# Kernel tuning notes

Measured on AMD Instinct MI355X. Metric: run time of the kernel, lower is better.

Reference implementation:

```python
import jax, jax.numpy as jnp
import numpy as np

B, T, D, HD = 8, 2048, 1024, 64

def setup_inputs() -> dict:
    key = jax.random.key(0)
    k1, k2, k3, k4 = jax.random.split(key, 4)
    x = jax.random.normal(k1, (B, T, D), dtype=jnp.float32)
    Wq = jax.random.normal(k2, (D, HD), dtype=jnp.float32) * (D ** -0.5)
    Wk = jax.random.normal(k3, (D, HD), dtype=jnp.float32) * (D ** -0.5)
    Wv = jax.random.normal(k4, (D, HD), dtype=jnp.float32) * (D ** -0.5)
    return {"x": x, "Wq": Wq, "Wk": Wk, "Wv": Wv}

def reference(x, Wq, Wk, Wv):
    # x: [B,T,D]; projections: [D,HD]
    q = jnp.einsum('btd,dh->bth', x, Wq)
    k = jnp.einsum('btd,dh->bth', x, Wk)
    v = jnp.einsum('btd,dh->bth', x, Wv)
    hd = q.shape[-1]
    scores = jnp.einsum('bth,bsh->bts', q, k) * (hd ** -0.5)  # [B,T,T]
    t = scores.shape[-1]
    causal = jnp.tril(jnp.ones((t, t), dtype=bool))
    scores = jnp.where(causal, scores, -jnp.inf)
    w = jax.nn.softmax(scores, axis=-1)
    # dropout p=0.0 (eval) -> identity
    return jnp.einsum('bts,bsh->bth', w, v)
```

## Files before the change

kernel.cpp:

```cpp
#include <hip/hip_runtime.h>
#include <hip/hip_bf16.h>
#include <stdint.h>

#define NB 8
#define TT 2048
#define DD 1024
#define HDIM 64

typedef __bf16 bf16x8 __attribute__((ext_vector_type(8)));
typedef float f32x4 __attribute__((ext_vector_type(4)));
typedef ushort u16x4 __attribute__((ext_vector_type(4)));

static_assert(sizeof(bf16x8) == 16, "bf16x8 must be 16 bytes");

__device__ inline ushort f2bf_bits(float f) {
    __hip_bfloat16 h = __float2bfloat16(f);
    return *reinterpret_cast<ushort*>(&h);
}
__device__ inline float bfbits2f(ushort u) {
    unsigned v = ((unsigned)u) << 16;
    return __builtin_bit_cast(float, v);
}
__device__ inline bf16x8 ldb8(const ushort* p) {
    return *reinterpret_cast<const bf16x8*>(p);
}

typedef __attribute__((address_space(3))) uint32_t lds_u32;
typedef const __attribute__((address_space(1))) uint32_t glb_u32;
__device__ inline void gl_lds16(const void* g, void* l) {
    __builtin_amdgcn_global_load_lds((glb_u32*)g, (lds_u32*)l, 16, 0, 0);
}

#define WCNT_VM2   0xF72
#define WCNT_VM5   0xF75
#define WCNT_LGKM0 0xC07F

__device__ inline int probe_f32(const ushort* x) {
    int lane = threadIdx.x & 63;
    int wild = 0;
    #pragma unroll
    for (int j = 0; j < 4; ++j) {
        ushort u = x[(lane * 4 + j) * 32];
        int e = (u >> 7) & 0xFF;
        wild += (e >= 0xC0);
    }
    unsigned long long m = __ballot(wild > 0);
    return __popcll(m) > 8;
}

__global__ __launch_bounds__(256) void k_wt(const ushort* __restrict__ x,
                                            const void* __restrict__ Wq,
                                            const void* __restrict__ Wk,
                                            const void* __restrict__ Wv,
                                            ushort* __restrict__ Wt) {
    int f32m = probe_f32(x);
    int idx = blockIdx.x * 256 + threadIdx.x;
    int mat = idx >> 16;
    int rem = idx & 65535;
    int d = rem >> 6;
    int h = rem & 63;
    const void* W = (mat == 0) ? Wq : (mat == 1) ? Wk : Wv;
    float v;
    if (f32m) v = ((const float*)W)[rem];
    else      v = bfbits2f(((const ushort*)W)[rem]);
    if (mat == 0) v *= 0.18033688011112042f;
    int n    = mat * 64 + h;
    int nt   = n >> 4, ncol = n & 15;
    int kk   = d >> 6, ks = (d >> 5) & 1, qd = (d >> 3) & 3, e = d & 7;
    int f    = nt * 2 + ks;
    Wt[((size_t)(kk * 24 + f)) * 512 + (qd * 16 + ncol) * 8 + e] = f2bf_bits(v);
}

template <int F32M>
__device__ inline void proj_body(const void* __restrict__ xv,
                                 const ushort* __restrict__ Wt,
                                 ushort* __restrict__ Qw,
                                 ushort* __restrict__ Kw,
                                 ushort* __restrict__ V2,
                                 ushort* Bf, ushort* Afb) {
    int tid  = threadIdx.x;
    int w    = tid >> 6;
    int lane = tid & 63;
    int quad = lane >> 4;
    int col  = lane & 15;
    int mtw  = w >> 2;
    int nh   = w & 3;
    int m0   = blockIdx.x * 64;

    const float*  xf = (const float*)xv;
    const ushort* xb = (const ushort*)xv;

    auto stageB = [&](int buf, int kkk) {
        int kk24 = (kkk >> 6) * 24;
        #pragma unroll
        for (int j = 0; j < 3; ++j) {
            int f = w * 3 + j;
            gl_lds16(Wt + ((size_t)(kk24 + f)) * 512 + lane * 8,
                     Bf + ((size_t)buf * 24 + f) * 512);
        }
    };

    int arow  = m0 + w * 8 + (lane >> 3);
    int amt_s = w >> 1;
    int colp  = (w & 1) * 8 + (lane >> 3);
    f32x4 arf[2];
    u16x4 arb[2];
    auto loadA = [&](int kkk) {
        #pragma unroll
        for (int i = 0; i < 2; ++i) {
            int c = (lane & 7) + i * 8;
            if (F32M) arf[i] = *reinterpret_cast<const f32x4*>(xf + (size_t)arow * DD + kkk + c * 4);
            else      arb[i] = *reinterpret_cast<const u16x4*>(xb + (size_t)arow * DD + kkk + c * 4);
        }
    };
    auto writeA = [&](int q) {
        #pragma unroll
        for (int i = 0; i < 2; ++i) {
            int c  = (lane & 7) + i * 8;
            int ks = i;
            int qd = (c & 7) >> 1;
            int e0 = (c & 1) * 4;
            u16x4 v;
            if (F32M) {
                #pragma unroll
                for (int j = 0; j < 4; ++j) v[j] = f2bf_bits(arf[i][j]);
            } else {
                v = arb[i];
            }
            *reinterpret_cast<u16x4*>(Afb + ((size_t)q * 16 + amt_s * 2 + ks) * 512
                                      + (qd * 16 + colp) * 8 + e0) = v;
        }
    };

    f32x4 acc[2][3];
    #pragma unroll
    for (int i = 0; i < 2; ++i)
        #pragma unroll
        for (int j = 0; j < 3; ++j) acc[i][j] = (f32x4){0.f, 0.f, 0.f, 0.f};

    loadA(0);
    stageB(0, 0);
    writeA(0);
    __builtin_amdgcn_s_waitcnt(WCNT_LGKM0);

    for (int t = 0; t < 16; ++t) {
        int p   = t & 1;
        int kn1 = (t + 1 < 16) ? (t + 1) * 64 : 960;
        loadA(kn1);
        stageB(p ^ 1, kn1);
        __builtin_amdgcn_s_waitcnt(WCNT_VM5);
        __builtin_amdgcn_s_barrier();

        #pragma unroll
        for (int ks = 0; ks < 2; ++ks) {
            bf16x8 a0 = ldb8(Afb + ((size_t)p * 16 + (mtw * 2 + 0) * 2 + ks) * 512 + lane * 8);
            bf16x8 a1 = ldb8(Afb + ((size_t)p * 16 + (mtw * 2 + 1) * 2 + ks) * 512 + lane * 8);
            #pragma unroll
            for (int j = 0; j < 3; ++j) {
                int nt = nh * 3 + j;
                bf16x8 b = ldb8(Bf + ((size_t)p * 24 + nt * 2 + ks) * 512 + lane * 8);
                acc[0][j] = __builtin_amdgcn_mfma_f32_16x16x32_bf16(a0, b, acc[0][j], 0, 0, 0);
                acc[1][j] = __builtin_amdgcn_mfma_f32_16x16x32_bf16(a1, b, acc[1][j], 0, 0, 0);
            }
        }
        writeA(p ^ 1);
        __builtin_amdgcn_s_waitcnt(WCNT_LGKM0);
        __builtin_amdgcn_s_barrier();
    }

    #pragma unroll
    for (int mloc = 0; mloc < 2; ++mloc) {
        #pragma unroll
        for (int j = 0; j < 3; ++j) {
            int nt  = nh * 3 + j;
            int mat = nt >> 2;
            int h   = (nt & 3) * 16 + col;
            if (mat == 2) {
                int row0 = m0 + mtw * 32 + mloc * 16 + quad * 4;
                int bb   = row0 >> 11;
                int t0   = row0 & (TT - 1);
                u16x4 v;
                #pragma unroll
                for (int r = 0; r < 4; ++r) v[r] = f2bf_bits(acc[mloc][j][r]);
                *reinterpret_cast<u16x4*>(V2 + (size_t)bb * HDIM * TT
                                          + (size_t)(t0 >> 5) * 2048
                                          + h * 32 + (t0 & 31)) = v;
            } else {
                ushort* outp = (mat == 0) ? Qw : Kw;
                #pragma unroll
                for (int r = 0; r < 4; ++r) {
                    int row = m0 + mtw * 32 + mloc * 16 + quad * 4 + r;
                    outp[(size_t)row * HDIM + h] = f2bf_bits(acc[mloc][j][r]);
                }
            }
        }
    }
}

__global__ __launch_bounds__(512, 4) void k_proj(const void* __restrict__ xv,
                                                 const ushort* __restrict__ Wt,
                                                 ushort* __restrict__ Qw,
                                                 ushort* __restrict__ Kw,
                                                 ushort* __restrict__ V2) {
    __shared__ ushort Bf[2 * 24 * 512];
    __shared__ ushort Afb[2 * 16 * 512];
    if (probe_f32((const ushort*)xv)) proj_body<1>(xv, Wt, Qw, Kw, V2, Bf, Afb);
    else                              proj_body<0>(xv, Wt, Qw, Kw, V2, Bf, Afb);
}

__global__ __launch_bounds__(256) void k_attn(const ushort* __restrict__ Qw,
                                              const ushort* __restrict__ Kw,
                                              const ushort* __restrict__ V2w,
                                              ushort* __restrict__ Po,
                                              float* __restrict__ Pl) {
    int w    = threadIdx.x >> 6;
    int lane = threadIdx.x & 63;
    int quad = lane >> 4;
    int col  = lane & 15;
    int bid  = blockIdx.x;
    int b    = bid & 7;
    int idx  = 79 - (bid >> 3);
    int c, g;
    if (idx < 32)      { c = 0; g = idx; }
    else if (idx < 56) { c = 1; g = idx - 24; }
    else if (idx < 72) { c = 2; g = idx - 40; }
    else               { c = 3; g = idx - 48; }
    int qb = 4 * g + w;
    int m0 = qb * 16;
    int Bq = (qb < 32) ? qb : (qb < 64) ? 2*qb - 32 : (qb < 96) ? 3*qb - 96 : 4*qb - 192;
    int pid = b * 320 + Bq + c;

    const ushort* Qb  = Qw  + (size_t)b * TT * HDIM;
    const ushort* Kb  = Kw  + (size_t)b * TT * HDIM;
    const ushort* V2b = V2w + (size_t)b * HDIM * TT;

    __shared__ ushort KVb[2][4096];
    __shared__ __hip_bfloat16 Pls[4][16][40];

    auto stageKV = [&](int buf, int s) {
        #pragma unroll
        for (int j = 0; j < 2; ++j) {
            int i = w * 2 + j;
            const ushort* gp;
            if (i < 4) {
                int row = i * 8 + (lane >> 3);
                int cg  = (lane & 7) ^ (lane >> 3);
                gp = Kb + (size_t)(s + row) * HDIM + cg * 8;
            } else {
                int w3 = (lane & 7) ^ (lane >> 3);
                int d  = (i - 4) * 16 + 2 * (lane >> 3) + (w3 >> 2);
                int cg = w3 & 3;
                gp = V2b + (size_t)(s >> 5) * 2048 + d * 32 + cg * 8;
            }
            gl_lds16(gp, &KVb[buf][i * 512]);
        }
    };

    int cb7  = col & 7;
    int vlow = (quad + 4 * (col & 1)) ^ ((col >> 1) & 7);
    auto kslot = [&](int rb, int half) {
        return ((rb + col) * 8 + ((half * 4 + quad) ^ cb7)) * 8;
    };
    auto vslot = [&](int vg) {
        return 2048 + ((vg * 8 + (col >> 1)) * 8 + vlow) * 8;
    };

    bf16x8 qf0 = ldb8(Qb + (size_t)(m0 + col) * HDIM + quad * 8);
    bf16x8 qf1 = ldb8(Qb + (size_t)(m0 + col) * HDIM + 32 + quad * 8);

    f32x4 o0 = {0.f,0.f,0.f,0.f};
    f32x4 o1 = {0.f,0.f,0.f,0.f};
    f32x4 o2 = {0.f,0.f,0.f,0.f};
    f32x4 o3 = {0.f,0.f,0.f,0.f};
    float rsum[4] = {0.f, 0.f, 0.f, 0.f};

    const int start = c * 512;
    const int end   = min(start + 512, 64 * g + 64);

    stageKV(0, start);
    for (int s0 = start; s0 < end; s0 += 32) {
        int p  = ((s0 - start) >> 5) & 1;
        int sn = (s0 + 32 < end) ? s0 + 32 : s0;
        stageKV(p ^ 1, sn);
        __builtin_amdgcn_s_waitcnt(WCNT_VM2);
        __builtin_amdgcn_s_barrier();

        if (s0 < m0 + 16) {
            bf16x8 ck0l = ldb8(&KVb[p][kslot(0,  0)]);
            bf16x8 ck0h = ldb8(&KVb[p][kslot(0,  1)]);
            bf16x8 ck1l = ldb8(&KVb[p][kslot(16, 0)]);
            bf16x8 ck1h = ldb8(&KVb[p][kslot(16, 1)]);

            f32x4 S0 = {0.f,0.f,0.f,0.f};
            f32x4 S1 = {0.f,0.f,0.f,0.f};
            S0 = __builtin_amdgcn_mfma_f32_16x16x32_bf16(qf0, ck0l, S0, 0, 0, 0);
            S0 = __builtin_amdgcn_mfma_f32_16x16x32_bf16(qf1, ck0h, S0, 0, 0, 0);
            S1 = __builtin_amdgcn_mfma_f32_16x16x32_bf16(qf0, ck1l, S1, 0, 0, 0);
            S1 = __builtin_amdgcn_mfma_f32_16x16x32_bf16(qf1, ck1h, S1, 0, 0, 0);

            #pragma unroll
            for (int r = 0; r < 4; ++r) {
                int trow = m0 + quad * 4 + r;
                float aa = (s0 + col      > trow) ? -1e30f : S0[r];
                float dd = (s0 + 16 + col > trow) ? -1e30f : S1[r];
                float p0 = exp2f(aa);
                float p1 = exp2f(dd);
                rsum[r] += p0 + p1;
                Pls[w][quad * 4 + r][col]      = __float2bfloat16(p0);
                Pls[w][quad * 4 + r][16 + col] = __float2bfloat16(p1);
            }
            bf16x8 pf = *reinterpret_cast<const bf16x8*>(&Pls[w][col][quad * 8]);

            bf16x8 cv0 = ldb8(&KVb[p][vslot(0)]);
            bf16x8 cv1 = ldb8(&KVb[p][vslot(1)]);
            bf16x8 cv2 = ldb8(&KVb[p][vslot(2)]);
            bf16x8 cv3 = ldb8(&KVb[p][vslot(3)]);
            o0 = __builtin_amdgcn_mfma_f32_16x16x32_bf16(pf, cv0, o0, 0, 0, 0);
            o1 = __builtin_amdgcn_mfma_f32_16x16x32_bf16(pf, cv1, o1, 0, 0, 0);
            o2 = __builtin_amdgcn_mfma_f32_16x16x32_bf16(pf, cv2, o2, 0, 0, 0);
            o3 = __builtin_amdgcn_mfma_f32_16x16x32_bf16(pf, cv3, o3, 0, 0, 0);
        }
        __builtin_amdgcn_s_waitcnt(WCNT_LGKM0);
        __builtin_amdgcn_s_barrier();
    }

    #pragma unroll
    for (int off = 1; off < 16; off <<= 1) {
        #pragma unroll
        for (int r = 0; r < 4; ++r)
            rsum[r] += __shfl_xor(rsum[r], off, 64);
    }

    ushort* pb = Po + (size_t)pid * 1024;
    #pragma unroll
    for (int r = 0; r < 4; ++r) {
        int row = quad * 4 + r;
        pb[row * 64 + 0*16 + col] = f2bf_bits(o0[r]);
        pb[row * 64 + 1*16 + col] = f2bf_bits(o1[r]);
        pb[row * 64 + 2*16 + col] = f2bf_bits(o2[r]);
        pb[row * 64 + 3*16 + col] = f2bf_bits(o3[r]);
        if (col == 0) Pl[pid * 16 + row] = rsum[r];
    }
}

__global__ __launch_bounds__(256) void k_merge(const ushort* __restrict__ x,
                                               const ushort* __restrict__ Po,
                                               const float* __restrict__ Pl,
                                               void* __restrict__ outv) {
    int f32m = probe_f32(x);
    int wid  = blockIdx.x * 4 + (threadIdx.x >> 6);
    int lane = threadIdx.x & 63;
    int row  = lane >> 2;
    int g    = lane & 3;
    int b    = wid >> 7;
    int qb   = wid & 127;
    int nch  = (qb >> 5) + 1;
    int Bq   = (qb < 32) ? qb : (qb < 64) ? 2*qb - 32 : (qb < 96) ? 3*qb - 96 : 4*qb - 192;
    int pid0 = b * 320 + Bq;

    float L = 0.f;
    #pragma unroll
    for (int c = 0; c < 4; ++c)
        if (c < nch) L += Pl[(pid0 + c) * 16 + row];
    float inv = 1.0f / L;

    float o[16];
    #pragma unroll
    for (int j = 0; j < 16; ++j) o[j] = 0.f;
    #pragma unroll
    for (int c = 0; c < 4; ++c) {
        if (c < nch) {
            const ushort* p = Po + (size_t)(pid0 + c) * 1024 + row * 64 + g * 16;
            bf16x8 v0 = ldb8(p);
            bf16x8 v1 = ldb8(p + 8);
            #pragma unroll
            for (int j = 0; j < 8; ++j) {
                o[j]     += (float)v0[j];
                o[8 + j] += (float)v1[j];
            }
        }
    }

    size_t obase = ((size_t)b * TT + qb * 16 + row) * HDIM + g * 16;
    if (f32m) {
        float* ob = (float*)outv + obase;
        #pragma unroll
        for (int j = 0; j < 16; ++j) ob[j] = o[j] * inv;
    } else {
        ushort* ob = (ushort*)outv + obase;
        #pragma unroll
        for (int j = 0; j < 16; ++j) ob[j] = f2bf_bits(o[j] * inv);
    }
}

extern "C" void kernel_launch(void* const* d_in, const int* in_sizes, int n_in,
                              void* d_out, int out_size, void* d_ws, size_t ws_size,
                              hipStream_t stream) {
    const ushort* x = (const ushort*)d_in[0];
    ushort* Wt  = (ushort*)d_ws;
    ushort* Qw  = Wt + 3 * HDIM * DD;
    ushort* Kw  = Qw + (size_t)NB * TT * HDIM;
    ushort* V2  = Kw + (size_t)NB * TT * HDIM;
    ushort* Po  = V2 + (size_t)NB * TT * HDIM;
    float*  Pl  = (float*)(Po + (size_t)2560 * 1024);

    k_wt   <<<768, 256, 0, stream>>>(x, d_in[1], d_in[2], d_in[3], Wt);
    k_proj <<<256, 512, 0, stream>>>(d_in[0], Wt, Qw, Kw, V2);
    k_attn <<<640, 256, 0, stream>>>(Qw, Kw, V2, Po, Pl);
    k_merge<<<256, 256, 0, stream>>>(x, Po, Pl, d_out);
}
```

Baseline: 142.4 us.

## Fuse split-KV merge into attention kernel via atomic last-block reduction

Removes the separate merge kernel launch. Query blocks that have a single KV chunk now normalize and write the output directly. Multi-chunk blocks write their partials, bump an atomic counter, and the last-arriving wave reduces all chunks and writes the final output. This saves one kernel launch and the partial round-trip for single-chunk rows, at the cost of threadfences, atomics and a serialized tail reduction inside the attention kernel. The counters are zeroed in the weight-transform kernel.

```diff
diff --git a/kernel.cpp b/kernel.cpp
--- a/kernel.cpp
+++ b/kernel.cpp
@@ -52,9 +52,11 @@
                                             const void* __restrict__ Wq,
                                             const void* __restrict__ Wk,
                                             const void* __restrict__ Wv,
-                                            ushort* __restrict__ Wt) {
+                                            ushort* __restrict__ Wt,
+                                            int* __restrict__ cnt) {
     int f32m = probe_f32(x);
     int idx = blockIdx.x * 256 + threadIdx.x;
+    if (idx < 1024) cnt[idx] = 0;
     int mat = idx >> 16;
     int rem = idx & 65535;
     int d = rem >> 6;
@@ -208,11 +210,15 @@
     else                              proj_body<0>(xv, Wt, Qw, Kw, V2, Bf, Afb);
 }
 
-__global__ __launch_bounds__(256) void k_attn(const ushort* __restrict__ Qw,
+__global__ __launch_bounds__(256) void k_attn(const ushort* __restrict__ xp,
+                                              const ushort* __restrict__ Qw,
                                               const ushort* __restrict__ Kw,
                                               const ushort* __restrict__ V2w,
                                               ushort* __restrict__ Po,
-                                              float* __restrict__ Pl) {
+                                              float* __restrict__ Pl,
+                                              int* __restrict__ cnt,
+                                              void* __restrict__ outv) {
+    int f32m = probe_f32(xp);
     int w    = threadIdx.x >> 6;
     int lane = threadIdx.x & 63;
     int quad = lane >> 4;
@@ -227,8 +233,10 @@
     else               { c = 3; g = idx - 48; }
     int qb = 4 * g + w;
     int m0 = qb * 16;
+    int nch = (qb >> 5) + 1;
     int Bq = (qb < 32) ? qb : (qb < 64) ? 2*qb - 32 : (qb < 96) ? 3*qb - 96 : 4*qb - 192;
-    int pid = b * 320 + Bq + c;
+    int pid0 = b * 320 + Bq;
+    int pid  = pid0 + c;
 
     const ushort* Qb  = Qw  + (size_t)b * TT * HDIM;
     const ushort* Kb  = Kw  + (size_t)b * TT * HDIM;
@@ -331,65 +339,77 @@
             rsum[r] += __shfl_xor(rsum[r], off, 64);
     }
 
-    ushort* pb = Po + (size_t)pid * 1024;
-    #pragma unroll
-    for (int r = 0; r < 4; ++r) {
-        int row = quad * 4 + r;
-        pb[row * 64 + 0*16 + col] = f2bf_bits(o0[r]);
-        pb[row * 64 + 1*16 + col] = f2bf_bits(o1[r]);
-        pb[row * 64 + 2*16 + col] = f2bf_bits(o2[r]);
-        pb[row * 64 + 3*16 + col] = f2bf_bits(o3[r]);
-        if (col == 0) Pl[pid * 16 + row] = rsum[r];
-    }
-}
-
-__global__ __launch_bounds__(256) void k_merge(const ushort* __restrict__ x,
-                                               const ushort* __restrict__ Po,
-                                               const float* __restrict__ Pl,
-                                               void* __restrict__ outv) {
-    int f32m = probe_f32(x);
-    int wid  = blockIdx.x * 4 + (threadIdx.x >> 6);
-    int lane = threadIdx.x & 63;
-    int row  = lane >> 2;
-    int g    = lane & 3;
-    int b    = wid >> 7;
-    int qb   = wid & 127;
-    int nch  = (qb >> 5) + 1;
-    int Bq   = (qb < 32) ? qb : (qb < 64) ? 2*qb - 32 : (qb < 96) ? 3*qb - 96 : 4*qb - 192;
-    int pid0 = b * 320 + Bq;
-
-    float L = 0.f;
-    #pragma unroll
-    for (int c = 0; c < 4; ++c)
-        if (c < nch) L += Pl[(pid0 + c) * 16 + row];
-    float inv = 1.0f / L;
-
-    float o[16];
-    #pragma unroll
-    for (int j = 0; j < 16; ++j) o[j] = 0.f;
-    #pragma unroll
-    for (int c = 0; c < 4; ++c) {
-        if (c < nch) {
-            const ushort* p = Po + (size_t)(pid0 + c) * 1024 + row * 64 + g * 16;
-            bf16x8 v0 = ldb8(p);
-            bf16x8 v1 = ldb8(p + 8);
+    if (nch == 1) {
+        size_t base = ((size_t)b * TT + (size_t)m0) * HDIM;
+        #pragma unroll
+        for (int r = 0; r < 4; ++r) {
+            float inv = 1.0f / rsum[r];
+            size_t ro = base + (size_t)(quad * 4 + r) * HDIM;
+            if (f32m) {
+                float* ob = (float*)outv;
+                ob[ro + 0*16 + col] = o0[r] * inv;
+                ob[ro + 1*16 + col] = o1[r] * inv;
+                ob[ro + 2*16 + col] = o2[r] * inv;
+                ob[ro + 3*16 + col] = o3[r] * inv;
+            } else {
+                ushort* ob = (ushort*)outv;
+                ob[ro + 0*16 + col] = f2bf_bits(o0[r] * inv);
+                ob[ro + 1*16 + col] = f2bf_bits(o1[r] * inv);
+                ob[ro + 2*16 + col] = f2bf_bits(o2[r] * inv);
+                ob[ro + 3*16 + col] = f2bf_bits(o3[r] * inv);
+            }
+        }
+    } else {
+        ushort* pb = Po + (size_t)pid * 1024;
+        #pragma unroll
+        for (int r = 0; r < 4; ++r) {
+            int row = quad * 4 + r;
+            pb[row * 64 + 0*16 + col] = f2bf_bits(o0[r]);
+            pb[row * 64 + 1*16 + col] = f2bf_bits(o1[r]);
+            pb[row * 64 + 2*16 + col] = f2bf_bits(o2[r]);
+            pb[row * 64 + 3*16 + col] = f2bf_bits(o3[r]);
+            if (col == 0) Pl[pid * 16 + row] = rsum[r];
+        }
+        __threadfence();
+        int old = 0;
+        if (lane == 0) old = atomicAdd(cnt + (b * 128 + qb), 1);
+        old = __shfl(old, 0, 64);
+        if (old == nch - 1) {
+            __threadfence();
+            int row = lane >> 2;
+            int gs  = lane & 3;
+            float L = 0.f;
             #pragma unroll
-            for (int j = 0; j < 8; ++j) {
-                o[j]     += (float)v0[j];
-                o[8 + j] += (float)v1[j];
-            }
-        }
-    }
-
-    size_t obase = ((size_t)b * TT + qb * 16 + row) * HDIM + g * 16;
-    if (f32m) {
-        float* ob = (float*)outv + obase;
-        #pragma unroll
-        for (int j = 0; j < 16; ++j) ob[j] = o[j] * inv;
-    } else {
-        ushort* ob = (ushort*)outv + obase;
-        #pragma unroll
-        for (int j = 0; j < 16; ++j) ob[j] = f2bf_bits(o[j] * inv);
+            for (int c2 = 0; c2 < 4; ++c2)
+                if (c2 < nch) L += Pl[(pid0 + c2) * 16 + row];
+            float inv = 1.0f / L;
+            float o[16];
+            #pragma unroll
+            for (int j = 0; j < 16; ++j) o[j] = 0.f;
+            #pragma unroll
+            for (int c2 = 0; c2 < 4; ++c2) {
+                if (c2 < nch) {
+                    const ushort* p = Po + (size_t)(pid0 + c2) * 1024 + row * 64 + gs * 16;
+                    bf16x8 v0 = ldb8(p);
+                    bf16x8 v1 = ldb8(p + 8);
+                    #pragma unroll
+                    for (int j = 0; j < 8; ++j) {
+                        o[j]     += (float)v0[j];
+                        o[8 + j] += (float)v1[j];
+                    }
+                }
+            }
+            size_t obase = ((size_t)b * TT + (size_t)m0 + row) * HDIM + gs * 16;
+            if (f32m) {
+                float* ob = (float*)outv + obase;
+                #pragma unroll
+                for (int j = 0; j < 16; ++j) ob[j] = o[j] * inv;
+            } else {
+                ushort* ob = (ushort*)outv + obase;
+                #pragma unroll
+                for (int j = 0; j < 16; ++j) ob[j] = f2bf_bits(o[j] * inv);
+            }
+        }
     }
 }
 
@@ -403,9 +423,9 @@
     ushort* V2  = Kw + (size_t)NB * TT * HDIM;
     ushort* Po  = V2 + (size_t)NB * TT * HDIM;
     float*  Pl  = (float*)(Po + (size_t)2560 * 1024);
-
-    k_wt   <<<768, 256, 0, stream>>>(x, d_in[1], d_in[2], d_in[3], Wt);
+    int*    cnt = (int*)(Pl + 2560 * 16);
+
+    k_wt   <<<768, 256, 0, stream>>>(x, d_in[1], d_in[2], d_in[3], Wt, cnt);
     k_proj <<<256, 512, 0, stream>>>(d_in[0], Wt, Qw, Kw, V2);
-    k_attn <<<640, 256, 0, stream>>>(Qw, Kw, V2, Po, Pl);
-    k_merge<<<256, 256, 0, stream>>>(x, Po, Pl, d_out);
-}
+    k_attn <<<640, 256, 0, stream>>>(x, Qw, Kw, V2, Po, Pl, cnt, d_out);
+}
```

Measured after the change: 225.1 us. 1.58x slower.
